# Optimization experiments

Hardware: AMD Instinct MI355X
Metric: run time of the kernel (lower is better)

Reference implementation:

```python
import jax, jax.numpy as jnp
import numpy as np

N_NODES = 100000
N_EDGES = 1600000
IN_FEAT = 128
OUT_FEAT = 64
RRELU_SLOPE = (1.0 / 8.0 + 1.0 / 3.0) / 2.0  # nn.RReLU eval-mode slope = 11/48


def setup_inputs() -> dict:
    key = jax.random.key(0)
    k1, k2, k3, k4, k5 = jax.random.split(key, 5)
    feat = jax.random.normal(k1, (N_NODES, IN_FEAT), dtype=jnp.float32)
    src = jax.random.randint(k2, (N_EDGES,), 0, N_NODES, dtype=jnp.int64)
    dst = jax.random.randint(k3, (N_EDGES,), 0, N_NODES, dtype=jnp.int64)
    # xavier-uniform-ish init
    b1 = np.sqrt(6.0 / (IN_FEAT + OUT_FEAT))
    b2 = np.sqrt(6.0 / (OUT_FEAT + OUT_FEAT))
    w1 = jax.random.uniform(k4, (IN_FEAT, OUT_FEAT), jnp.float32, -b1, b1)
    w2 = jax.random.uniform(k5, (OUT_FEAT, OUT_FEAT), jnp.float32, -b2, b2)
    return {"feat": feat, "src": src, "dst": dst, "w1": w1, "w2": w2}


def _gather_sum(h, src, dst):
    # DGL copy_src('h','m') + sum: for each dst node, sum messages from src nodes
    return jax.ops.segment_sum(h[src], dst, num_segments=N_NODES)


def _rrelu(x):
    return jnp.where(x >= 0, x, RRELU_SLOPE * x)


def reference(feat, src, dst, w1, w2):
    # pattern = 0: linear -> gather -> rrelu, linear -> gather -> rrelu
    h = feat @ w1                      # [N, out_feat]
    h = _gather_sum(h, src, dst)       # [N, out_feat]
    h = _rrelu(h)
    h = h @ w2                         # [N, out_feat]
    h = _gather_sum(h, src, dst)       # [N, out_feat]
    h = _rrelu(h)
    return h
```

## Files before the change

kernel.cpp:

```cpp
#include <hip/hip_runtime.h>

#define N_NODES 100000
#define N_EDGES 1600000
#define IN_FEAT 128
#define OUT_FEAT 64
#define SLOPE 0.22916666666666666f

#define NPB 128
#define NB 782
#define CAP 2560
#define BIN_CHUNK 8192
#define EPT 32
#define BIN_BLOCKS ((N_EDGES + BIN_CHUNK - 1) / BIN_CHUNK)
#define GEMM1_BLOCKS (N_NODES / 16)

__device__ __forceinline__ ushort f2bf(float x) {
    unsigned u = __float_as_uint(x);
    u += 0x7FFFu + ((u >> 16) & 1u);
    return (ushort)(u >> 16);
}

union FatSmem {
    struct { float w[IN_FEAT * OUT_FEAT]; float f[16 * IN_FEAT]; } g;
    struct { int cnt[NB]; int gbase[NB]; } b;
};

__global__ __launch_bounds__(256) void gemm1_binning_kernel(
        const float* __restrict__ feat, const float* __restrict__ w1,
        ushort* __restrict__ h1,
        const int* __restrict__ src, const int* __restrict__ dst,
        int* __restrict__ bcur, int* __restrict__ pairs) {
    __shared__ FatSmem s;
    const int tid = threadIdx.x;

    if (blockIdx.x >= BIN_BLOCKS) {
        float* w = s.g.w;
        float* f = s.g.f;
        const float4* w4 = (const float4*)w1;
        float4* wl = (float4*)w;
#pragma unroll
        for (int i = 0; i < 8; ++i) wl[tid + i * 256] = w4[tid + i * 256];

        const int row0 = (blockIdx.x - BIN_BLOCKS) * 16;
        const float4* fg = (const float4*)(feat + (size_t)row0 * IN_FEAT);
        float4* fl = (float4*)f;
#pragma unroll
        for (int i = 0; i < 2; ++i) fl[tid + i * 256] = fg[tid + i * 256];
        __syncthreads();

        const int c = tid & 63;
        const int rg = tid >> 6;
        float acc0 = 0.f, acc1 = 0.f, acc2 = 0.f, acc3 = 0.f;
        const float4* fv = (const float4*)f;
#pragma unroll
        for (int k = 0; k < IN_FEAT; k += 4) {
            const float wa = w[(k + 0) * OUT_FEAT + c];
            const float wb = w[(k + 1) * OUT_FEAT + c];
            const float wc = w[(k + 2) * OUT_FEAT + c];
            const float wd = w[(k + 3) * OUT_FEAT + c];
            float4 a = fv[((rg * 4 + 0) * IN_FEAT + k) >> 2];
            acc0 += a.x * wa + a.y * wb + a.z * wc + a.w * wd;
            float4 bb = fv[((rg * 4 + 1) * IN_FEAT + k) >> 2];
            acc1 += bb.x * wa + bb.y * wb + bb.z * wc + bb.w * wd;
            float4 d = fv[((rg * 4 + 2) * IN_FEAT + k) >> 2];
            acc2 += d.x * wa + d.y * wb + d.z * wc + d.w * wd;
            float4 e = fv[((rg * 4 + 3) * IN_FEAT + k) >> 2];
            acc3 += e.x * wa + e.y * wb + e.z * wc + e.w * wd;
        }
        h1[(size_t)(row0 + rg * 4 + 0) * OUT_FEAT + c] = f2bf(acc0);
        h1[(size_t)(row0 + rg * 4 + 1) * OUT_FEAT + c] = f2bf(acc1);
        h1[(size_t)(row0 + rg * 4 + 2) * OUT_FEAT + c] = f2bf(acc2);
        h1[(size_t)(row0 + rg * 4 + 3) * OUT_FEAT + c] = f2bf(acc3);
    } else {
        int* cnt = s.b.cnt;
        int* gbase = s.b.gbase;
        for (int i = tid; i < NB; i += 256) cnt[i] = 0;
        __syncthreads();
        const int base = blockIdx.x * BIN_CHUNK;
        int bl[EPT];
        int vp[EPT];
#pragma unroll
        for (int i = 0; i < EPT; ++i) {
            const int e = base + i * 256 + tid;
            if (e < N_EDGES) {
                const int d = dst[e];
                const int b = d >> 7;
                const int lpos = atomicAdd(&cnt[b], 1);
                bl[i] = (b << 13) | lpos;
                vp[i] = ((d & 127) << 17) | src[e];
            } else {
                bl[i] = -1;
            }
        }
        __syncthreads();
        for (int i = tid; i < NB; i += 256) {
            const int c = cnt[i];
            gbase[i] = c ? (i * CAP + atomicAdd(&bcur[i], c)) : 0;
        }
        __syncthreads();
#pragma unroll
        for (int i = 0; i < EPT; ++i) {
            if (bl[i] >= 0) {
                const int b = bl[i] >> 13, lpos = bl[i] & 8191;
                pairs[gbase[b] + lpos] = vp[i];
            }
        }
    }
}

__global__ __launch_bounds__(256) void sort2_kernel(const int* __restrict__ pairs,
                                                    const int* __restrict__ bcur,
                                                    int* __restrict__ csr,
                                                    int2* __restrict__ nseg) {
    __shared__ int cnt[NPB];
    __shared__ int cur[NPB];
    __shared__ int wtot;
    const int b = blockIdx.x;
    const int t = threadIdx.x;
    const int beg = b * CAP;
    const int end = beg + bcur[b];
    if (t < NPB) cnt[t] = 0;
    __syncthreads();
    for (int i = beg + t; i < end; i += 256)
        atomicAdd(&cnt[pairs[i] >> 17], 1);
    __syncthreads();
    int v = 0, x = 0;
    const int lane = t & 63, w = t >> 6;
    if (t < NPB) {
        v = cnt[t];
        x = v;
#pragma unroll
        for (int off = 1; off < 64; off <<= 1) {
            int y = __shfl_up(x, off);
            if (lane >= off) x += y;
        }
        if (t == 63) wtot = x;
    }
    __syncthreads();
    if (t < NPB) {
        const int gp = beg + (x - v) + (w ? wtot : 0);
        cur[t] = gp;
        nseg[b * NPB + t] = make_int2(gp, gp + v);
    }
    __syncthreads();
    for (int i = beg + t; i < end; i += 256) {
        const int p = pairs[i];
        const int pos = atomicAdd(&cur[p >> 17], 1);
        csr[pos] = (p & 0x1FFFF) << 7;
    }
}

__device__ __forceinline__ float2 gather_pairs(const char* __restrict__ hb,
                                               const int* __restrict__ csr,
                                               int beg, int end, int hi, int cp4) {
    float ax = 0.f, ay = 0.f;
    int i = beg;
#define LOADU(k) const unsigned u##k = *(const unsigned*)(hb + (unsigned)(csr[i + 2*(k) + hi] + cp4))
#define ACCU(k)                                            \
    ax += __uint_as_float(u##k << 16);                     \
    ay += __uint_as_float(u##k & 0xFFFF0000u)
    for (; i + 16 <= end; i += 16) {
        LOADU(0); LOADU(1); LOADU(2); LOADU(3);
        LOADU(4); LOADU(5); LOADU(6); LOADU(7);
        ACCU(0); ACCU(1); ACCU(2); ACCU(3);
        ACCU(4); ACCU(5); ACCU(6); ACCU(7);
    }
    if (i + 8 <= end) {
        LOADU(0); LOADU(1); LOADU(2); LOADU(3);
        ACCU(0); ACCU(1); ACCU(2); ACCU(3);
        i += 8;
    }
    if (i + 4 <= end) {
        LOADU(0); LOADU(1);
        ACCU(0); ACCU(1);
        i += 4;
    }
    for (; i < end; i += 2) {
        if (i + hi < end) {
            const unsigned u = *(const unsigned*)(hb + (unsigned)(csr[i + hi] + cp4));
            ax += __uint_as_float(u << 16);
            ay += __uint_as_float(u & 0xFFFF0000u);
        }
    }
#undef LOADU
#undef ACCU
    return make_float2(ax, ay);
}

__global__ __launch_bounds__(256) void agg_gemm2_kernel(const ushort* __restrict__ h,
                                                        const int* __restrict__ csr,
                                                        const int2* __restrict__ nseg,
                                                        const float* __restrict__ w2,
                                                        ushort* __restrict__ h2) {
    __shared__ float w[OUT_FEAT * OUT_FEAT];
    __shared__ float rowbuf[4][OUT_FEAT];
    const int tid = threadIdx.x;

    const float4* w4g = (const float4*)w2;
    float4* wl = (float4*)w;
#pragma unroll
    for (int i = 0; i < 4; ++i) wl[tid + i * 256] = w4g[tid + i * 256];
    __syncthreads();

    const int wv = tid >> 6, c = tid & 63;
    const int hi = (tid >> 5) & 1, cp = tid & 31;
    const int node = blockIdx.x * 4 + wv;
    const int2 seg = nseg[node];

    float2 acc = gather_pairs((const char*)h, csr, seg.x, seg.y, hi, cp * 4);
    acc.x += __shfl_xor(acc.x, 32);
    acc.y += __shfl_xor(acc.y, 32);
    acc.x = acc.x >= 0.f ? acc.x : acc.x * SLOPE;
    acc.y = acc.y >= 0.f ? acc.y : acc.y * SLOPE;

    if (hi == 0) ((float2*)rowbuf[wv])[cp] = acc;

    float o = 0.f;
    const float4* rb4 = (const float4*)rowbuf[wv];
#pragma unroll
    for (int k = 0; k < OUT_FEAT; k += 4) {
        const float4 r = rb4[k >> 2];
        o += r.x * w[(k + 0) * OUT_FEAT + c] + r.y * w[(k + 1) * OUT_FEAT + c] +
             r.z * w[(k + 2) * OUT_FEAT + c] + r.w * w[(k + 3) * OUT_FEAT + c];
    }
    h2[(size_t)node * OUT_FEAT + c] = f2bf(o);
}

__global__ __launch_bounds__(256) void agg_rrelu_kernel(const ushort* __restrict__ h,
                                                        const int* __restrict__ csr,
                                                        const int2* __restrict__ nseg,
                                                        float* __restrict__ out) {
    const int tid = threadIdx.x;
    const int hi = (tid >> 5) & 1, cp = tid & 31;
    const int node = blockIdx.x * 4 + (tid >> 6);
    const int2 seg = nseg[node];

    float2 acc = gather_pairs((const char*)h, csr, seg.x, seg.y, hi, cp * 4);
    acc.x += __shfl_xor(acc.x, 32);
    acc.y += __shfl_xor(acc.y, 32);
    if (hi == 0) {
        acc.x = acc.x >= 0.f ? acc.x : acc.x * SLOPE;
        acc.y = acc.y >= 0.f ? acc.y : acc.y * SLOPE;
        ((float2*)(out + (size_t)node * OUT_FEAT))[cp] = acc;
    }
}

extern "C" void kernel_launch(void* const* d_in, const int* in_sizes, int n_in,
                              void* d_out, int out_size, void* d_ws, size_t ws_size,
                              hipStream_t stream) {
    const float* feat = (const float*)d_in[0];
    const int*   src  = (const int*)d_in[1];
    const int*   dst  = (const int*)d_in[2];
    const float* w1   = (const float*)d_in[3];
    const float* w2   = (const float*)d_in[4];
    float* out = (float*)d_out;

    ushort* h1   = (ushort*)d_ws;
    ushort* h2   = h1 + (size_t)N_NODES * OUT_FEAT;
    int*    pairs = (int*)h2;
    int*    csr  = (int*)(h2 + (size_t)N_NODES * OUT_FEAT);
    int2*   nseg = (int2*)(csr + NB * CAP);
    int*    bcur = (int*)(nseg + NB * NPB);

    hipMemsetAsync(bcur, 0, NB * sizeof(int), stream);
    gemm1_binning_kernel<<<BIN_BLOCKS + GEMM1_BLOCKS, 256, 0, stream>>>(
        feat, w1, h1, src, dst, bcur, pairs);
    sort2_kernel<<<NB, 256, 0, stream>>>(pairs, bcur, csr, nseg);

    agg_gemm2_kernel<<<N_NODES / 4, 256, 0, stream>>>(h1, csr, nseg, w2, h2);

    agg_rrelu_kernel<<<N_NODES / 4, 256, 0, stream>>>(h2, csr, nseg, out);
}
```

Before: 174.8 us.

## Split GEMM1 over K with register-held weights and make segment bounds wave-uniform

The GEMM1 blocks no longer stage the whole 128x64 W1 tile in shared memory. Each wave now keeps a 32-row K-slice of W1 in registers, computes partial sums for all 16 rows, and reduces the four partials through shared memory before writing packed bf16 pairs. This cuts LDS footprint and shared-memory weight traffic, which may raise occupancy, at the cost of more registers and an extra reduction pass. Separately, the aggregation kernels broadcast segment begin/end with readfirstlane so the gather loop bounds become scalar and uniform across the wave.

After: 167.5 us. 4.2% less time.

```diff
diff --git a/kernel.cpp b/kernel.cpp
--- a/kernel.cpp
+++ b/kernel.cpp
@@ -21,7 +21,7 @@
 }
 
 union FatSmem {
-    struct { float w[IN_FEAT * OUT_FEAT]; float f[16 * IN_FEAT]; } g;
+    struct { float f[16 * IN_FEAT]; float part[4 * 16 * OUT_FEAT]; } g;
     struct { int cnt[NB]; int gbase[NB]; } b;
 };
 
@@ -34,43 +34,53 @@
     const int tid = threadIdx.x;
 
     if (blockIdx.x >= BIN_BLOCKS) {
-        float* w = s.g.w;
-        float* f = s.g.f;
-        const float4* w4 = (const float4*)w1;
-        float4* wl = (float4*)w;
-#pragma unroll
-        for (int i = 0; i < 8; ++i) wl[tid + i * 256] = w4[tid + i * 256];
+        const int c = tid & 63;
+        const int ks = tid >> 6;
+
+        float wr[32];
+#pragma unroll
+        for (int j = 0; j < 32; ++j)
+            wr[j] = w1[(ks * 32 + j) * OUT_FEAT + c];
 
         const int row0 = (blockIdx.x - BIN_BLOCKS) * 16;
         const float4* fg = (const float4*)(feat + (size_t)row0 * IN_FEAT);
-        float4* fl = (float4*)f;
-#pragma unroll
-        for (int i = 0; i < 2; ++i) fl[tid + i * 256] = fg[tid + i * 256];
-        __syncthreads();
-
-        const int c = tid & 63;
-        const int rg = tid >> 6;
-        float acc0 = 0.f, acc1 = 0.f, acc2 = 0.f, acc3 = 0.f;
-        const float4* fv = (const float4*)f;
-#pragma unroll
-        for (int k = 0; k < IN_FEAT; k += 4) {
-            const float wa = w[(k + 0) * OUT_FEAT + c];
-            const float wb = w[(k + 1) * OUT_FEAT + c];
-            const float wc = w[(k + 2) * OUT_FEAT + c];
-            const float wd = w[(k + 3) * OUT_FEAT + c];
-            float4 a = fv[((rg * 4 + 0) * IN_FEAT + k) >> 2];
-            acc0 += a.x * wa + a.y * wb + a.z * wc + a.w * wd;
-            float4 bb = fv[((rg * 4 + 1) * IN_FEAT + k) >> 2];
-            acc1 += bb.x * wa + bb.y * wb + bb.z * wc + bb.w * wd;
-            float4 d = fv[((rg * 4 + 2) * IN_FEAT + k) >> 2];
-            acc2 += d.x * wa + d.y * wb + d.z * wc + d.w * wd;
-            float4 e = fv[((rg * 4 + 3) * IN_FEAT + k) >> 2];
-            acc3 += e.x * wa + e.y * wb + e.z * wc + e.w * wd;
-        }
-        h1[(size_t)(row0 + rg * 4 + 0) * OUT_FEAT + c] = f2bf(acc0);
-        h1[(size_t)(row0 + rg * 4 + 1) * OUT_FEAT + c] = f2bf(acc1);
-        h1[(size_t)(row0 + rg * 4 + 2) * OUT_FEAT + c] = f2bf(acc2);
-        h1[(size_t)(row0 + rg * 4 + 3) * OUT_FEAT + c] = f2bf(acc3);
+        float4* fl = (float4*)s.g.f;
+        fl[tid] = fg[tid];
+        fl[tid + 256] = fg[tid + 256];
+        __syncthreads();
+
+        float acc[16];
+#pragma unroll
+        for (int r = 0; r < 16; ++r) acc[r] = 0.f;
+
+        const float4* fv = (const float4*)s.g.f;
+#pragma unroll
+        for (int j4 = 0; j4 < 8; ++j4) {
+            const float wa = wr[4 * j4], wb = wr[4 * j4 + 1];
+            const float wc = wr[4 * j4 + 2], wd = wr[4 * j4 + 3];
+#pragma unroll
+            for (int r = 0; r < 16; ++r) {
+                const float4 a = fv[r * 32 + ks * 8 + j4];
+                acc[r] += a.x * wa + a.y * wb + a.z * wc + a.w * wd;
+            }
+        }
+
+#pragma unroll
+        for (int r = 0; r < 16; ++r)
+            s.g.part[ks * (16 * OUT_FEAT) + r * OUT_FEAT + c] = acc[r];
+        __syncthreads();
+
+        ushort2* h1u2 = (ushort2*)h1;
+#pragma unroll
+        for (int half = 0; half < 2; ++half) {
+            const int idx = half * 256 + tid;
+            const int r = idx >> 5;
+            const int cp = idx & 31;
+            const float* p = s.g.part + r * OUT_FEAT + 2 * cp;
+            const float lo = p[0] + p[1024] + p[2048] + p[3072];
+            const float hi = p[1] + p[1025] + p[2049] + p[3073];
+            h1u2[(size_t)(row0 + r) * 32 + cp] = make_ushort2(f2bf(lo), f2bf(hi));
+        }
     } else {
         int* cnt = s.b.cnt;
         int* gbase = s.b.gbase;
@@ -94,8 +104,8 @@
         }
         __syncthreads();
         for (int i = tid; i < NB; i += 256) {
-            const int c = cnt[i];
-            gbase[i] = c ? (i * CAP + atomicAdd(&bcur[i], c)) : 0;
+            const int cc = cnt[i];
+            gbase[i] = cc ? (i * CAP + atomicAdd(&bcur[i], cc)) : 0;
         }
         __syncthreads();
 #pragma unroll
@@ -206,8 +216,10 @@
     const int hi = (tid >> 5) & 1, cp = tid & 31;
     const int node = blockIdx.x * 4 + wv;
     const int2 seg = nseg[node];
-
-    float2 acc = gather_pairs((const char*)h, csr, seg.x, seg.y, hi, cp * 4);
+    const int beg = __builtin_amdgcn_readfirstlane(seg.x);
+    const int end = __builtin_amdgcn_readfirstlane(seg.y);
+
+    float2 acc = gather_pairs((const char*)h, csr, beg, end, hi, cp * 4);
     acc.x += __shfl_xor(acc.x, 32);
     acc.y += __shfl_xor(acc.y, 32);
     acc.x = acc.x >= 0.f ? acc.x : acc.x * SLOPE;
@@ -234,8 +246,10 @@
     const int hi = (tid >> 5) & 1, cp = tid & 31;
     const int node = blockIdx.x * 4 + (tid >> 6);
     const int2 seg = nseg[node];
-
-    float2 acc = gather_pairs((const char*)h, csr, seg.x, seg.y, hi, cp * 4);
+    const int beg = __builtin_amdgcn_readfirstlane(seg.x);
+    const int end = __builtin_amdgcn_readfirstlane(seg.y);
+
+    float2 acc = gather_pairs((const char*)h, csr, beg, end, hi, cp * 4);
     acc.x += __shfl_xor(acc.x, 32);
     acc.y += __shfl_xor(acc.y, 32);
     if (hi == 0) {
```
